# Optimization experiments

Measured on AMD Instinct MI355X. Metric: run time of the kernel, lower is better.

Reference implementation:

```python
import jax, jax.numpy as jnp
import numpy as np

STATE_MASS = 4.0
EPS = 1e-5
LOW_RANK_SCALE = 0.1  # _LOW_RANK_SCALE_INIT


def _ln(x, g, b):
    mu = jnp.mean(x, axis=-1, keepdims=True)
    var = jnp.var(x, axis=-1, keepdims=True)
    return (x - mu) * jax.lax.rsqrt(var + EPS) * g + b


def _signed_abs_softmax(s, axis=-1):
    s = jnp.nan_to_num(s)
    return jnp.sign(s) * jax.nn.softmax(jnp.abs(s), axis=axis)


def _signed_softmax_state(st):
    st = jnp.nan_to_num(st)
    return jnp.sign(st) * jax.nn.softmax(jnp.abs(st), axis=-1) * STATE_MASS


def _low_rank_scores(dst, src, Ut_w, Ut_b, Us_w, Us_b, w):
    # bilinear low-rank pairwise: score[b,i,j] = sum_r (dst_i Ut)_r * w_r * (src_j Us)_r
    pt = dst @ Ut_w + Ut_b                      # [B,Nd,R]
    ps = src @ Us_w + Us_b                      # [B,Ns,R]
    return jnp.einsum('bir,r,bjr->bij', pt, w * LOW_RANK_SCALE, ps)


def _gather_rows(x, idx):
    # x: [B,N,...], idx: [B,M,K] -> [B,M,K,...] (per-batch gather, no NxM broadcast)
    return jax.vmap(lambda xi, ii: xi[ii])(x, idx)


def setup_inputs() -> dict:
    key = jax.random.key(0)
    ks = jax.random.split(key, 8)
    B, S, D, M, R = 16, 2048, 512, 256, 64
    std = 0.02
    return {
        'token_val': jax.random.normal(ks[0], (B, S, D), jnp.float32),
        'token_state': jax.random.normal(ks[1], (B, S), jnp.float32),
        'init_state': jax.random.normal(ks[2], (M,), jnp.float32) * std,
        'init_val': jax.random.normal(ks[3], (M, D), jnp.float32) * std,
        'rUs_w': jax.random.normal(ks[4], (D, R), jnp.float32) * std,
        'rUs_b': jnp.zeros((R,), jnp.float32),
        'rUt_w': jax.random.normal(ks[5], (D, R), jnp.float32) * std,
        'rUt_b': jnp.zeros((R,), jnp.float32),
        'r_w': jnp.ones((R,), jnp.float32),
        'pUs_w': jax.random.normal(ks[6], (D, R), jnp.float32) * std,
        'pUs_b': jnp.zeros((R,), jnp.float32),
        'pUt_w': jax.random.normal(ks[7], (D, R), jnp.float32) * std,
        'pUt_b': jnp.zeros((R,), jnp.float32),
        'p_w': jnp.ones((R,), jnp.float32),
        'ln_g': jnp.ones((D,), jnp.float32),
        'ln_b': jnp.zeros((D,), jnp.float32),
        'topk': 16,
    }


def reference(token_val, token_state, init_state, init_val,
              rUs_w, rUs_b, rUt_w, rUt_b, r_w,
              pUs_w, pUs_b, pUt_w, pUt_b, p_w,
              ln_g, ln_b, topk):
    B = token_val.shape[0]
    M, D = init_val.shape

    # _MemoryLevel.initialize
    mem_state = _signed_softmax_state(jnp.broadcast_to(init_state, (B, M)))
    mem_val = _ln(jnp.broadcast_to(init_val, (B, M, D)), ln_g, ln_b)

    # ---- SparseTransition (write): route tokens -> slots, top-k sources/slot ----
    scores = _low_rank_scores(mem_val, token_val, rUt_w, rUt_b, rUs_w, rUs_b, r_w)  # [B,M,S]
    _, idx = jax.lax.top_k(jnp.abs(scores), topk)              # [B,M,K]
    sel = jnp.take_along_axis(scores, idx, axis=-1)            # [B,M,K]
    edges = _signed_abs_softmax(sel, axis=-1)                  # signed-abs-softmax over edges
    v_sel = _gather_rows(token_val, idx)                       # [B,M,K,D]
    s_sel = _gather_rows(token_state, idx)                     # [B,M,K]
    mem_val = mem_val + jnp.einsum('bmk,bmkd->bmd', edges, v_sel)   # merge_mode='add'
    mem_state = mem_state + jnp.einsum('bmk,bmk->bm', edges, s_sel)
    mem_state = _signed_softmax_state(mem_state)
    mem_val = _ln(mem_val, ln_g, ln_b)

    # ---- SparsePropagation within slots: state-weighted top-k edges, residual ----
    pscores = _low_rank_scores(mem_val, mem_val, pUt_w, pUt_b, pUs_w, pUs_b, p_w)   # [B,M,M]
    pscores = pscores * mem_state[:, None, :]                  # state_weight_edges
    _, pidx = jax.lax.top_k(jnp.abs(pscores), topk)            # [B,M,K]
    psel = jnp.take_along_axis(pscores, pidx, axis=-1)
    pe = _signed_abs_softmax(psel, axis=-1)
    pv = _gather_rows(mem_val, pidx)                           # [B,M,K,D]
    pst = _gather_rows(mem_state, pidx)                        # [B,M,K]
    mem_val = mem_val + jnp.einsum('bmk,bmkd->bmd', pe, pv)    # residual=True
    mem_state = mem_state + jnp.einsum('bmk,bmk->bm', pe, pst)
    mem_state = _signed_softmax_state(mem_state)
    mem_val = _ln(mem_val, ln_g, ln_b)
    return mem_val
```

## Files before the change

kernel.cpp:

```cpp
#include <hip/hip_runtime.h>
#include <hip/hip_bf16.h>
#include <math.h>

#define BB 16
#define SS 2048
#define DD 512
#define MM 256
#define RR 64
#define KK 16
#define GPAD 68

__device__ __forceinline__ float wave_sum(float v) {
#pragma unroll
  for (int off = 32; off > 0; off >>= 1) v += __shfl_xor(v, off);
  return v;
}

__device__ __forceinline__ float sgnf(float v) {
  return (v > 0.f) ? 1.f : ((v < 0.f) ? -1.f : 0.f);
}

__global__ __launch_bounds__(256) void k_init(
    const float* __restrict__ init_val, const float* __restrict__ ln_g,
    const float* __restrict__ ln_b, const float* __restrict__ rUt_w,
    const float* __restrict__ rUt_b, const float* __restrict__ r_w,
    float* __restrict__ mv0, float* __restrict__ pt0) {
  int m = blockIdx.x, t = threadIdx.x;
  __shared__ float row[DD];
  __shared__ float red[8];
  float x0 = init_val[m * DD + t];
  float x1 = init_val[m * DD + t + 256];
  float s = wave_sum(x0 + x1);
  float sq = wave_sum(x0 * x0 + x1 * x1);
  if ((t & 63) == 0) { red[t >> 6] = s; red[4 + (t >> 6)] = sq; }
  __syncthreads();
  float mean = (red[0] + red[1] + red[2] + red[3]) * (1.0f / DD);
  float var = (red[4] + red[5] + red[6] + red[7]) * (1.0f / DD) - mean * mean;
  float rs = rsqrtf(var + 1e-5f);
  float n0 = (x0 - mean) * rs * ln_g[t] + ln_b[t];
  float n1 = (x1 - mean) * rs * ln_g[t + 256] + ln_b[t + 256];
  mv0[m * DD + t] = n0;
  mv0[m * DD + t + 256] = n1;
  row[t] = n0;
  row[t + 256] = n1;
  __syncthreads();
  if (t < RR) {
    float acc = rUt_b[t];
    for (int d = 0; d < DD; ++d) acc += row[d] * rUt_w[d * RR + t];
    pt0[m * RR + t] = acc * r_w[t] * 0.1f;
  }
}

__global__ __launch_bounds__(256) void k_state_softmax(
    const float* __restrict__ in, float* __restrict__ out) {
  int b = blockIdx.x, t = threadIdx.x;
  __shared__ float red[4];
  float v = in[b * MM + t];
  float a = fabsf(v);
  float mx = a;
#pragma unroll
  for (int off = 32; off > 0; off >>= 1) mx = fmaxf(mx, __shfl_xor(mx, off));
  if ((t & 63) == 0) red[t >> 6] = mx;
  __syncthreads();
  mx = fmaxf(fmaxf(red[0], red[1]), fmaxf(red[2], red[3]));
  __syncthreads();
  float e = expf(a - mx);
  float ssum = wave_sum(e);
  if ((t & 63) == 0) red[t >> 6] = ssum;
  __syncthreads();
  ssum = red[0] + red[1] + red[2] + red[3];
  out[b * MM + t] = sgnf(v) * e / ssum * 4.0f;
}

__global__ __launch_bounds__(256) void k_ps(
    const float* __restrict__ A, const float* __restrict__ W,
    const float* __restrict__ bias, float* __restrict__ C) {
  __shared__ float Ast[32][128];
  __shared__ float Ws[32][RR];
  int t = threadIdx.x;
  int tx = t & 15;
  int ty = t >> 4;
  int row0 = blockIdx.x * 128;
  float4 ra[4];
  float4 rw[2];
#pragma unroll
  for (int i = 0; i < 4; ++i) {
    int slot = i * 256 + t;
    int r = slot >> 3, k4 = slot & 7;
    ra[i] = *reinterpret_cast<const float4*>(&A[(size_t)(row0 + r) * DD + k4 * 4]);
  }
#pragma unroll
  for (int i = 0; i < 2; ++i) {
    int slot = i * 256 + t;
    int k = slot >> 4, c4 = slot & 15;
    rw[i] = *reinterpret_cast<const float4*>(&W[(size_t)k * RR + c4 * 4]);
  }
  float acc[8][4] = {};
  for (int c = 0; c < 16; ++c) {
    __syncthreads();
#pragma unroll
    for (int i = 0; i < 4; ++i) {
      int slot = i * 256 + t;
      int r = slot >> 3, k4 = slot & 7;
      Ast[k4 * 4 + 0][r] = ra[i].x;
      Ast[k4 * 4 + 1][r] = ra[i].y;
      Ast[k4 * 4 + 2][r] = ra[i].z;
      Ast[k4 * 4 + 3][r] = ra[i].w;
    }
#pragma unroll
    for (int i = 0; i < 2; ++i) {
      int slot = i * 256 + t;
      int k = slot >> 4, c4 = slot & 15;
      *reinterpret_cast<float4*>(&Ws[k][c4 * 4]) = rw[i];
    }
    __syncthreads();
    if (c < 15) {
      int kc = (c + 1) * 32;
#pragma unroll
      for (int i = 0; i < 4; ++i) {
        int slot = i * 256 + t;
        int r = slot >> 3, k4 = slot & 7;
        ra[i] = *reinterpret_cast<const float4*>(
            &A[(size_t)(row0 + r) * DD + kc + k4 * 4]);
      }
#pragma unroll
      for (int i = 0; i < 2; ++i) {
        int slot = i * 256 + t;
        int k = slot >> 4, c4 = slot & 15;
        rw[i] = *reinterpret_cast<const float4*>(
            &W[(size_t)(kc + k) * RR + c4 * 4]);
      }
    }
#pragma unroll
    for (int k = 0; k < 32; ++k) {
      float4 alo = *reinterpret_cast<const float4*>(&Ast[k][ty * 8]);
      float4 ahi = *reinterpret_cast<const float4*>(&Ast[k][ty * 8 + 4]);
      float4 w4 = *reinterpret_cast<const float4*>(&Ws[k][tx * 4]);
      acc[0][0] += alo.x * w4.x; acc[0][1] += alo.x * w4.y; acc[0][2] += alo.x * w4.z; acc[0][3] += alo.x * w4.w;
      acc[1][0] += alo.y * w4.x; acc[1][1] += alo.y * w4.y; acc[1][2] += alo.y * w4.z; acc[1][3] += alo.y * w4.w;
      acc[2][0] += alo.z * w4.x; acc[2][1] += alo.z * w4.y; acc[2][2] += alo.z * w4.z; acc[2][3] += alo.z * w4.w;
      acc[3][0] += alo.w * w4.x; acc[3][1] += alo.w * w4.y; acc[3][2] += alo.w * w4.z; acc[3][3] += alo.w * w4.w;
      acc[4][0] += ahi.x * w4.x; acc[4][1] += ahi.x * w4.y; acc[4][2] += ahi.x * w4.z; acc[4][3] += ahi.x * w4.w;
      acc[5][0] += ahi.y * w4.x; acc[5][1] += ahi.y * w4.y; acc[5][2] += ahi.y * w4.z; acc[5][3] += ahi.y * w4.w;
      acc[6][0] += ahi.z * w4.x; acc[6][1] += ahi.z * w4.y; acc[6][2] += ahi.z * w4.z; acc[6][3] += ahi.z * w4.w;
      acc[7][0] += ahi.w * w4.x; acc[7][1] += ahi.w * w4.y; acc[7][2] += ahi.w * w4.z; acc[7][3] += ahi.w * w4.w;
    }
  }
  float4 bv = *reinterpret_cast<const float4*>(&bias[tx * 4]);
#pragma unroll
  for (int r = 0; r < 8; ++r) {
    int rr = row0 + ty * 8 + r;
    float4 o;
    o.x = acc[r][0] + bv.x; o.y = acc[r][1] + bv.y;
    o.z = acc[r][2] + bv.z; o.w = acc[r][3] + bv.w;
    *reinterpret_cast<float4*>(&C[(size_t)rr * RR + tx * 4]) = o;
  }
}

template <bool TRANS_OUT>
__device__ __forceinline__ void gemm_body(
    const float* __restrict__ A, const float* __restrict__ W,
    const float* __restrict__ bias, const float* __restrict__ colscale,
    float csmul, const float* __restrict__ rowscale, float* __restrict__ C,
    int row0, float (*Ast)[GPAD], float (*Ws)[GPAD]) {
  int tid = threadIdx.x;
  int ty = tid >> 4, tx = tid & 15;
  float acc[4][4] = {};
  for (int kc = 0; kc < DD; kc += 32) {
#pragma unroll
    for (int i = 0; i < 2; ++i) {
      int s4 = i * 256 + tid;
      int r = s4 >> 3;
      int k4 = s4 & 7;
      float4 v = *reinterpret_cast<const float4*>(
          &A[(size_t)(row0 + r) * DD + kc + k4 * 4]);
      Ast[k4 * 4 + 0][r] = v.x;
      Ast[k4 * 4 + 1][r] = v.y;
      Ast[k4 * 4 + 2][r] = v.z;
      Ast[k4 * 4 + 3][r] = v.w;
    }
#pragma unroll
    for (int i = 0; i < 2; ++i) {
      int s4 = i * 256 + tid;
      int r = s4 >> 4;
      int c4 = s4 & 15;
      float4 v = *reinterpret_cast<const float4*>(
          &W[(size_t)(kc + r) * RR + c4 * 4]);
      *reinterpret_cast<float4*>(&Ws[r][c4 * 4]) = v;
    }
    __syncthreads();
#pragma unroll
    for (int k = 0; k < 32; ++k) {
      float4 a4 = *reinterpret_cast<const float4*>(&Ast[k][ty * 4]);
      float4 w4 = *reinterpret_cast<const float4*>(&Ws[k][tx * 4]);
      acc[0][0] += a4.x * w4.x; acc[0][1] += a4.x * w4.y;
      acc[0][2] += a4.x * w4.z; acc[0][3] += a4.x * w4.w;
      acc[1][0] += a4.y * w4.x; acc[1][1] += a4.y * w4.y;
      acc[1][2] += a4.y * w4.z; acc[1][3] += a4.y * w4.w;
      acc[2][0] += a4.z * w4.x; acc[2][1] += a4.z * w4.y;
      acc[2][2] += a4.z * w4.z; acc[2][3] += a4.z * w4.w;
      acc[3][0] += a4.w * w4.x; acc[3][1] += a4.w * w4.y;
      acc[3][2] += a4.w * w4.z; acc[3][3] += a4.w * w4.w;
    }
    __syncthreads();
  }
#pragma unroll
  for (int i = 0; i < 4; ++i) {
    int rr = row0 + ty * 4 + i;
    float rsc = rowscale ? rowscale[rr] : 1.f;
#pragma unroll
    for (int j = 0; j < 4; ++j) {
      int cc = tx * 4 + j;
      float v = acc[i][j] + bias[cc];
      if (colscale) v *= colscale[cc] * csmul;
      v *= rsc;
      if (TRANS_OUT) {
        C[((size_t)(rr >> 8) * RR + cc) * MM + (rr & 255)] = v;
      } else {
        C[(size_t)rr * RR + cc] = v;
      }
    }
  }
}

__global__ __launch_bounds__(256) void k_gemm_pair(
    const float* __restrict__ mv1, const float* __restrict__ pUt_w,
    const float* __restrict__ pUt_b, const float* __restrict__ p_w,
    const float* __restrict__ pUs_w, const float* __restrict__ pUs_b,
    const float* __restrict__ ms1, float* __restrict__ pt1,
    float* __restrict__ ps1T) {
  __shared__ float Ast[32][GPAD];
  __shared__ float Ws[32][GPAD];
  if (blockIdx.x < 64) {
    gemm_body<false>(mv1, pUt_w, pUt_b, p_w, 0.1f, nullptr, pt1,
                     blockIdx.x * 64, Ast, Ws);
  } else {
    gemm_body<true>(mv1, pUs_w, pUs_b, nullptr, 1.f, ms1, ps1T,
                    (blockIdx.x - 64) * 64, Ast, Ws);
  }
}

#define PSW 144
__device__ __forceinline__ int psw(int j) { return j + ((j >> 5) << 2); }

__global__ __launch_bounds__(256) void k_scores(
    const float* __restrict__ pt0, const float* __restrict__ ps,
    float* __restrict__ scores) {
  __shared__ float PtT[RR][64];
  __shared__ float PsT[RR][PSW];
  int t = threadIdx.x;
  int b = blockIdx.z;
  int m0 = blockIdx.y * 64;
  int j0 = blockIdx.x * 128;
  {
    int tm4 = t >> 4, tk4 = t & 15;
    const float* base = pt0 + (size_t)(m0 + tm4 * 4) * RR + tk4 * 4;
    float4 v0 = *reinterpret_cast<const float4*>(base);
    float4 v1 = *reinterpret_cast<const float4*>(base + RR);
    float4 v2 = *reinterpret_cast<const float4*>(base + 2 * RR);
    float4 v3 = *reinterpret_cast<const float4*>(base + 3 * RR);
    float4 w;
    w.x = v0.x; w.y = v1.x; w.z = v2.x; w.w = v3.x;
    *reinterpret_cast<float4*>(&PtT[tk4 * 4 + 0][tm4 * 4]) = w;
    w.x = v0.y; w.y = v1.y; w.z = v2.y; w.w = v3.y;
    *reinterpret_cast<float4*>(&PtT[tk4 * 4 + 1][tm4 * 4]) = w;
    w.x = v0.z; w.y = v1.z; w.z = v2.z; w.w = v3.z;
    *reinterpret_cast<float4*>(&PtT[tk4 * 4 + 2][tm4 * 4]) = w;
    w.x = v0.w; w.y = v1.w; w.z = v2.w; w.w = v3.w;
    *reinterpret_cast<float4*>(&PtT[tk4 * 4 + 3][tm4 * 4]) = w;
  }
#pragma unroll
  for (int ii = 0; ii < 2; ++ii) {
    int slot = ii * 256 + t;
    int jt = slot >> 4, kt = slot & 15;
    const float* base = ps + ((size_t)b * SS + j0 + jt * 4) * RR + kt * 4;
    float4 v0 = *reinterpret_cast<const float4*>(base);
    float4 v1 = *reinterpret_cast<const float4*>(base + RR);
    float4 v2 = *reinterpret_cast<const float4*>(base + 2 * RR);
    float4 v3 = *reinterpret_cast<const float4*>(base + 3 * RR);
    int jc = psw(jt * 4);
    float4 w;
    w.x = v0.x; w.y = v1.x; w.z = v2.x; w.w = v3.x;
    *reinterpret_cast<float4*>(&PsT[kt * 4 + 0][jc]) = w;
    w.x = v0.y; w.y = v1.y; w.z = v2.y; w.w = v3.y;
    *reinterpret_cast<float4*>(&PsT[kt * 4 + 1][jc]) = w;
    w.x = v0.z; w.y = v1.z; w.z = v2.z; w.w = v3.z;
    *reinterpret_cast<float4*>(&PsT[kt * 4 + 2][jc]) = w;
    w.x = v0.w; w.y = v1.w; w.z = v2.w; w.w = v3.w;
    *reinterpret_cast<float4*>(&PsT[kt * 4 + 3][jc]) = w;
  }
  __syncthreads();
  int tj = t & 15;
  int tm = t >> 4;
  int jlo = psw(tj * 8);
  int jhi = psw(tj * 8 + 4);
  float acc[4][8] = {};
#pragma unroll
  for (int k = 0; k < RR; ++k) {
    float4 a4 = *reinterpret_cast<const float4*>(&PtT[k][tm * 4]);
    float4 w0 = *reinterpret_cast<const float4*>(&PsT[k][jlo]);
    float4 w1 = *reinterpret_cast<const float4*>(&PsT[k][jhi]);
    acc[0][0] += a4.x * w0.x; acc[0][1] += a4.x * w0.y; acc[0][2] += a4.x * w0.z; acc[0][3] += a4.x * w0.w;
    acc[0][4] += a4.x * w1.x; acc[0][5] += a4.x * w1.y; acc[0][6] += a4.x * w1.z; acc[0][7] += a4.x * w1.w;
    acc[1][0] += a4.y * w0.x; acc[1][1] += a4.y * w0.y; acc[1][2] += a4.y * w0.z; acc[1][3] += a4.y * w0.w;
    acc[1][4] += a4.y * w1.x; acc[1][5] += a4.y * w1.y; acc[1][6] += a4.y * w1.z; acc[1][7] += a4.y * w1.w;
    acc[2][0] += a4.z * w0.x; acc[2][1] += a4.z * w0.y; acc[2][2] += a4.z * w0.z; acc[2][3] += a4.z * w0.w;
    acc[2][4] += a4.z * w1.x; acc[2][5] += a4.z * w1.y; acc[2][6] += a4.z * w1.z; acc[2][7] += a4.z * w1.w;
    acc[3][0] += a4.w * w0.x; acc[3][1] += a4.w * w0.y; acc[3][2] += a4.w * w0.z; acc[3][3] += a4.w * w0.w;
    acc[3][4] += a4.w * w1.x; acc[3][5] += a4.w * w1.y; acc[3][6] += a4.w * w1.z; acc[3][7] += a4.w * w1.w;
  }
  float* obase = scores + (size_t)b * MM * SS + (size_t)(m0 + tm * 4) * SS + j0 + tj * 8;
#pragma unroll
  for (int i = 0; i < 4; ++i) {
    float4 o0, o1;
    o0.x = acc[i][0]; o0.y = acc[i][1]; o0.z = acc[i][2]; o0.w = acc[i][3];
    o1.x = acc[i][4]; o1.y = acc[i][5]; o1.z = acc[i][6]; o1.w = acc[i][7];
    *reinterpret_cast<float4*>(obase + (size_t)i * SS) = o0;
    *reinterpret_cast<float4*>(obase + (size_t)i * SS + 4) = o1;
  }
}

__global__ __launch_bounds__(256) void k_write(
    const float* __restrict__ scores, const float* __restrict__ token_val,
    const float* __restrict__ token_state, const float* __restrict__ mv0,
    const float* __restrict__ ms0, const float* __restrict__ ln_g,
    const float* __restrict__ ln_b, float* __restrict__ mv1,
    float* __restrict__ ms_w) {
  int t = threadIdx.x;
  int wave = t >> 6, lane = t & 63;
  int i = blockIdx.x;
  int slot = i >> 3;
  int b = 2 * (i & 7) + (slot >> 6);
  int m = (slot & 63) * 4 + wave;
  int row = b * MM + m;
  __shared__ float srl[4][SS];
  __shared__ int selj_sh[4][KK];
  float4* srl4 = reinterpret_cast<float4*>(&srl[wave][0]);
  const float* srow = scores + (size_t)row * SS;
  unsigned maxa = 0u;
#pragma unroll
  for (int ch = 0; ch < 8; ++ch) {
    float4 q = *reinterpret_cast<const float4*>(srow + (ch * 64 + lane) * 4);
    srl4[ch * 64 + lane] = q;
    maxa = max(maxa, __float_as_uint(q.x) & 0x7fffffffu);
    maxa = max(maxa, __float_as_uint(q.y) & 0x7fffffffu);
    maxa = max(maxa, __float_as_uint(q.z) & 0x7fffffffu);
    maxa = max(maxa, __float_as_uint(q.w) & 0x7fffffffu);
  }
#pragma unroll
  for (int off = 32; off > 0; off >>= 1)
    maxa = max(maxa, (unsigned)__shfl_xor((int)maxa, off));
  unsigned lo = 0u, hi = maxa, thr = 0u;
  bool early = false;
  while (lo < hi) {
    unsigned mid = lo + ((hi - lo + 1u) >> 1);
    int cnt = 0;
#pragma unroll
    for (int ch = 0; ch < 8; ++ch) {
      float4 q = srl4[ch * 64 + lane];
      cnt += __popcll(__ballot((__float_as_uint(q.x) & 0x7fffffffu) >= mid));
      cnt += __popcll(__ballot((__float_as_uint(q.y) & 0x7fffffffu) >= mid));
      cnt += __popcll(__ballot((__float_as_uint(q.z) & 0x7fffffffu) >= mid));
      cnt += __popcll(__ballot((__float_as_uint(q.w) & 0x7fffffffu) >= mid));
    }
    if (cnt == KK) { thr = mid; early = true; break; }
    if (cnt > KK) lo = mid; else hi = mid - 1u;
  }
  if (!early) thr = lo;
  unsigned long long ltmask = (1ull << lane) - 1ull;
  int s = 0;
  unsigned tiemask = 0u;
#pragma unroll
  for (int ch = 0; ch < 8; ++ch) {
    float4 q = srl4[ch * 64 + lane];
    unsigned a4[4] = {__float_as_uint(q.x) & 0x7fffffffu,
                      __float_as_uint(q.y) & 0x7fffffffu,
                      __float_as_uint(q.z) & 0x7fffffffu,
                      __float_as_uint(q.w) & 0x7fffffffu};
#pragma unroll
    for (int cc = 0; cc < 4; ++cc) {
      bool sg = early ? (a4[cc] >= thr) : (a4[cc] > thr);
      unsigned long long mk = __ballot(sg);
      if (sg) selj_sh[wave][s + __popcll(mk & ltmask)] = ch * 256 + lane * 4 + cc;
      s += __popcll(mk);
      if (!early && a4[cc] == thr) tiemask |= 1u << (ch * 4 + cc);
    }
  }
  int taken = s;
  while (taken < KK) {
    int myj = 0x7fffffff;
#pragma unroll
    for (int c = 0; c < 32; ++c)
      if ((tiemask >> c) & 1u) {
        int j = (c >> 2) * 256 + lane * 4 + (c & 3);
        myj = min(myj, j);
      }
    int wj = myj;
#pragma unroll
    for (int off = 32; off > 0; off >>= 1) wj = min(wj, __shfl_xor(wj, off));
    if (wj == 0x7fffffff) break;
    if (((wj >> 2) & 63) == lane) tiemask &= ~(1u << (((wj >> 8) << 2) | (wj & 3)));
    if (lane == 0) selj_sh[wave][taken] = wj;
    ++taken;
  }
  int js[KK];
  float es[KK];
#pragma unroll
  for (int k = 0; k < KK; ++k) {
    js[k] = selj_sh[wave][k];
    es[k] = srl[wave][js[k]];
  }
  float mx = 0.f;
#pragma unroll
  for (int k = 0; k < KK; ++k) mx = fmaxf(mx, fabsf(es[k]));
  float ssum = 0.f;
#pragma unroll
  for (int k = 0; k < KK; ++k) {
    float ex = expf(fabsf(es[k]) - mx);
    ssum += ex;
    es[k] = sgnf(es[k]) * ex;
  }
  float inv = 1.f / ssum;
  int dbase = lane * 8;
  const float* m0row = mv0 + m * DD + dbase;
  float4 a0 = *reinterpret_cast<const float4*>(m0row);
  float4 a1 = *reinterpret_cast<const float4*>(m0row + 4);
  float acc[8] = {a0.x, a0.y, a0.z, a0.w, a1.x, a1.y, a1.z, a1.w};
  float stacc = 0.f;
#pragma unroll
  for (int k = 0; k < KK; ++k) {
    float e = es[k] * inv;
    const float* tv = token_val + ((size_t)b * SS + js[k]) * DD + dbase;
    float4 u0 = *reinterpret_cast<const float4*>(tv);
    float4 u1 = *reinterpret_cast<const float4*>(tv + 4);
    acc[0] += e * u0.x; acc[1] += e * u0.y; acc[2] += e * u0.z; acc[3] += e * u0.w;
    acc[4] += e * u1.x; acc[5] += e * u1.y; acc[6] += e * u1.z; acc[7] += e * u1.w;
    stacc += e * token_state[(size_t)b * SS + js[k]];
  }
  if (lane == 0) ms_w[row] = ms0[m] + stacc;
  float s1 = 0.f, s2 = 0.f;
#pragma unroll
  for (int c = 0; c < 8; ++c) { s1 += acc[c]; s2 += acc[c] * acc[c]; }
  s1 = wave_sum(s1);
  s2 = wave_sum(s2);
  float mean = s1 * (1.0f / DD);
  float var = s2 * (1.0f / DD) - mean * mean;
  float rs = rsqrtf(var + 1e-5f);
  float4 g0 = *reinterpret_cast<const float4*>(ln_g + dbase);
  float4 g1 = *reinterpret_cast<const float4*>(ln_g + dbase + 4);
  float4 b0v = *reinterpret_cast<const float4*>(ln_b + dbase);
  float4 b1v = *reinterpret_cast<const float4*>(ln_b + dbase + 4);
  float4 o0, o1;
  o0.x = (acc[0] - mean) * rs * g0.x + b0v.x;
  o0.y = (acc[1] - mean) * rs * g0.y + b0v.y;
  o0.z = (acc[2] - mean) * rs * g0.z + b0v.z;
  o0.w = (acc[3] - mean) * rs * g0.w + b0v.w;
  o1.x = (acc[4] - mean) * rs * g1.x + b1v.x;
  o1.y = (acc[5] - mean) * rs * g1.y + b1v.y;
  o1.z = (acc[6] - mean) * rs * g1.z + b1v.z;
  o1.w = (acc[7] - mean) * rs * g1.w + b1v.w;
  float* orow = mv1 + (size_t)row * DD + dbase;
  *reinterpret_cast<float4*>(orow) = o0;
  *reinterpret_cast<float4*>(orow + 4) = o1;
}

__global__ __launch_bounds__(256, 4) void k_prop(
    const float* __restrict__ pt1, const float* __restrict__ ps1T,
    const float* __restrict__ mv1, const float* __restrict__ ln_g,
    const float* __restrict__ ln_b, float* __restrict__ out) {
  int t = threadIdx.x;
  int wave = t >> 6, lane = t & 63;
  int row = blockIdx.x * 4 + wave;
  int b = row >> 8, m = row & 255;
  __shared__ int selj_sh[4][KK];
  __shared__ float selv_sh[4][KK];
  float ptval = pt1[(size_t)row * RR + lane];
  const float* pB = ps1T + (size_t)b * RR * MM + lane * 4;
  float sc[4] = {0.f, 0.f, 0.f, 0.f};
#pragma unroll 8
  for (int r = 0; r < RR; ++r) {
    float w = __shfl(ptval, r);
    float4 pv = *reinterpret_cast<const float4*>(pB + r * MM);
    sc[0] += w * pv.x; sc[1] += w * pv.y; sc[2] += w * pv.z; sc[3] += w * pv.w;
  }
  int jbase = lane * 4;
  unsigned au[4];
#pragma unroll
  for (int c = 0; c < 4; ++c) au[c] = __float_as_uint(sc[c]) & 0x7fffffffu;
  unsigned lo = 0u, hi = 0x7f800000u, thr = 0u;
  bool early = false;
  while (lo < hi) {
    unsigned mid = lo + ((hi - lo + 1u) >> 1);
    int cnt = 0;
#pragma unroll
    for (int c = 0; c < 4; ++c) cnt += __popcll(__ballot(au[c] >= mid));
    if (cnt == KK) { thr = mid; early = true; break; }
    if (cnt > KK) lo = mid; else hi = mid - 1u;
  }
  if (!early) thr = lo;
  unsigned long long ltmask = (1ull << lane) - 1ull;
  int s = 0;
  unsigned tiemask = 0u;
#pragma unroll
  for (int c = 0; c < 4; ++c) {
    bool sg = early ? (au[c] >= thr) : (au[c] > thr);
    unsigned long long mk = __ballot(sg);
    if (sg) {
      int slot = s + __popcll(mk & ltmask);
      selj_sh[wave][slot] = jbase + c;
      selv_sh[wave][slot] = sc[c];
    }
    s += __popcll(mk);
    if (!early && au[c] == thr) tiemask |= 1u << c;
  }
  int taken = s;
  while (taken < KK) {
    int myj = 0x7fffffff;
#pragma unroll
    for (int c = 0; c < 4; ++c)
      if ((tiemask >> c) & 1u) myj = min(myj, jbase + c);
    int wj = myj;
#pragma unroll
    for (int off = 32; off > 0; off >>= 1) wj = min(wj, __shfl_xor(wj, off));
    if (wj == 0x7fffffff) break;
    if (wj >= jbase && wj < jbase + 4) {
      tiemask &= ~(1u << (wj - jbase));
      selv_sh[wave][taken] = sc[wj - jbase];
      if (lane == (wj >> 2)) selj_sh[wave][taken] = wj;
    }
    ++taken;
  }
  int js[KK];
  float es[KK];
#pragma unroll
  for (int k = 0; k < KK; ++k) { js[k] = selj_sh[wave][k]; es[k] = selv_sh[wave][k]; }
  float mx = 0.f;
#pragma unroll
  for (int k = 0; k < KK; ++k) mx = fmaxf(mx, fabsf(es[k]));
  float ssum = 0.f;
#pragma unroll
  for (int k = 0; k < KK; ++k) {
    float ex = expf(fabsf(es[k]) - mx);
    ssum += ex;
    es[k] = sgnf(es[k]) * ex;
  }
  float inv = 1.f / ssum;
  int dbase = lane * 8;
  const float* mrow = mv1 + (size_t)row * DD + dbase;
  float4 a0 = *reinterpret_cast<const float4*>(mrow);
  float4 a1 = *reinterpret_cast<const float4*>(mrow + 4);
  float acc[8] = {a0.x, a0.y, a0.z, a0.w, a1.x, a1.y, a1.z, a1.w};
#pragma unroll
  for (int k = 0; k < KK; ++k) {
    float e = es[k] * inv;
    const float* pv = mv1 + ((size_t)b * MM + js[k]) * DD + dbase;
    float4 u0 = *reinterpret_cast<const float4*>(pv);
    float4 u1 = *reinterpret_cast<const float4*>(pv + 4);
    acc[0] += e * u0.x; acc[1] += e * u0.y; acc[2] += e * u0.z; acc[3] += e * u0.w;
    acc[4] += e * u1.x; acc[5] += e * u1.y; acc[6] += e * u1.z; acc[7] += e * u1.w;
  }
  float s1 = 0.f, s2 = 0.f;
#pragma unroll
  for (int c = 0; c < 8; ++c) { s1 += acc[c]; s2 += acc[c] * acc[c]; }
  s1 = wave_sum(s1);
  s2 = wave_sum(s2);
  float mean = s1 * (1.0f / DD);
  float var = s2 * (1.0f / DD) - mean * mean;
  float rs = rsqrtf(var + 1e-5f);
  float4 g0 = *reinterpret_cast<const float4*>(ln_g + dbase);
  float4 g1 = *reinterpret_cast<const float4*>(ln_g + dbase + 4);
  float4 b0v = *reinterpret_cast<const float4*>(ln_b + dbase);
  float4 b1v = *reinterpret_cast<const float4*>(ln_b + dbase + 4);
  float4 o0, o1;
  o0.x = (acc[0] - mean) * rs * g0.x + b0v.x;
  o0.y = (acc[1] - mean) * rs * g0.y + b0v.y;
  o0.z = (acc[2] - mean) * rs * g0.z + b0v.z;
  o0.w = (acc[3] - mean) * rs * g0.w + b0v.w;
  o1.x = (acc[4] - mean) * rs * g1.x + b1v.x;
  o1.y = (acc[5] - mean) * rs * g1.y + b1v.y;
  o1.z = (acc[6] - mean) * rs * g1.z + b1v.z;
  o1.w = (acc[7] - mean) * rs * g1.w + b1v.w;
  float* orow = out + (size_t)row * DD + dbase;
  *reinterpret_cast<float4*>(orow) = o0;
  *reinterpret_cast<float4*>(orow + 4) = o1;
}

extern "C" void kernel_launch(void* const* d_in, const int* in_sizes, int n_in,
                              void* d_out, int out_size, void* d_ws,
                              size_t ws_size, hipStream_t stream) {
  const float* token_val = (const float*)d_in[0];
  const float* token_state = (const float*)d_in[1];
  const float* init_state = (const float*)d_in[2];
  const float* init_val = (const float*)d_in[3];
  const float* rUs_w = (const float*)d_in[4];
  const float* rUs_b = (const float*)d_in[5];
  const float* rUt_w = (const float*)d_in[6];
  const float* rUt_b = (const float*)d_in[7];
  const float* r_w = (const float*)d_in[8];
  const float* pUs_w = (const float*)d_in[9];
  const float* pUs_b = (const float*)d_in[10];
  const float* pUt_w = (const float*)d_in[11];
  const float* pUt_b = (const float*)d_in[12];
  const float* p_w = (const float*)d_in[13];
  const float* ln_g = (const float*)d_in[14];
  const float* ln_b = (const float*)d_in[15];
  float* out = (float*)d_out;

  float* ws = (float*)d_ws;
  float* mv0 = ws;    ws += MM * DD;
  float* pt0 = ws;    ws += MM * RR;
  float* ms0 = ws;    ws += MM;
  float* ps = ws;     ws += (size_t)BB * SS * RR;
  float* scores = ws; ws += (size_t)BB * MM * SS;
  float* mv1 = ws;    ws += (size_t)BB * MM * DD;
  float* ms_w = ws;   ws += BB * MM;
  float* ms1 = ws;    ws += BB * MM;
  float* pt1 = ws;    ws += (size_t)BB * MM * RR;
  float* ps1T = ws;   ws += (size_t)BB * RR * MM;

  k_init<<<MM, 256, 0, stream>>>(init_val, ln_g, ln_b, rUt_w, rUt_b, r_w, mv0, pt0);
  k_state_softmax<<<1, 256, 0, stream>>>(init_state, ms0);
  k_ps<<<(BB * SS) / 128, 256, 0, stream>>>(token_val, rUs_w, rUs_b, ps);
  dim3 gs(SS / 128, MM / 64, BB);
  k_scores<<<gs, 256, 0, stream>>>(pt0, ps, scores);
  k_write<<<(BB * MM) / 4, 256, 0, stream>>>(scores, token_val, token_state,
                                             mv0, ms0, ln_g, ln_b, mv1, ms_w);
  k_state_softmax<<<BB, 256, 0, stream>>>(ms_w, ms1);
  k_gemm_pair<<<128, 256, 0, stream>>>(mv1, pUt_w, pUt_b, p_w, pUs_w, pUs_b,
                                       ms1, pt1, ps1T);
  k_prop<<<(BB * MM) / 4, 256, 0, stream>>>(pt1, ps1T, mv1, ln_g, ln_b, out);
}
```

Measured before the change: 173.8 us.

## Split k_ps reduction over two K halves and sum partials in k_scores

The token projection GEMM is split along the D dimension into two halves, doubling the grid from 256 to 512 blocks so more CUs are busy. The two partial results are written to separate buffers (the second reusing mv1 workspace) and summed when k_scores loads them. The A-tile load mapping is also changed so a wave reads consecutive rows instead of consecutive columns. The cost is an extra 8 MB partial buffer written and read, plus doubled loads in k_scores.

```diff
diff --git a/kernel.cpp b/kernel.cpp
--- a/kernel.cpp
+++ b/kernel.cpp
@@ -74,34 +74,41 @@
 
 __global__ __launch_bounds__(256) void k_ps(
     const float* __restrict__ A, const float* __restrict__ W,
-    const float* __restrict__ bias, float* __restrict__ C) {
+    const float* __restrict__ bias, float* __restrict__ C0,
+    float* __restrict__ C1) {
   __shared__ float Ast[32][128];
   __shared__ float Ws[32][RR];
   int t = threadIdx.x;
+  int lane = t & 63;
+  int wv = t >> 6;
   int tx = t & 15;
   int ty = t >> 4;
-  int row0 = blockIdx.x * 128;
+  int half = blockIdx.x >> 8;
+  int row0 = (blockIdx.x & 255) * 128;
+  int k0 = half * 256;
+  float* C = half ? C1 : C0;
   float4 ra[4];
   float4 rw[2];
 #pragma unroll
   for (int i = 0; i < 4; ++i) {
-    int slot = i * 256 + t;
-    int r = slot >> 3, k4 = slot & 7;
-    ra[i] = *reinterpret_cast<const float4*>(&A[(size_t)(row0 + r) * DD + k4 * 4]);
+    int r = (i & 1) * 64 + lane;
+    int k4 = (i >> 1) * 4 + wv;
+    ra[i] = *reinterpret_cast<const float4*>(
+        &A[(size_t)(row0 + r) * DD + k0 + k4 * 4]);
   }
 #pragma unroll
   for (int i = 0; i < 2; ++i) {
     int slot = i * 256 + t;
     int k = slot >> 4, c4 = slot & 15;
-    rw[i] = *reinterpret_cast<const float4*>(&W[(size_t)k * RR + c4 * 4]);
+    rw[i] = *reinterpret_cast<const float4*>(&W[(size_t)(k0 + k) * RR + c4 * 4]);
   }
   float acc[8][4] = {};
-  for (int c = 0; c < 16; ++c) {
+  for (int c = 0; c < 8; ++c) {
     __syncthreads();
 #pragma unroll
     for (int i = 0; i < 4; ++i) {
-      int slot = i * 256 + t;
-      int r = slot >> 3, k4 = slot & 7;
+      int r = (i & 1) * 64 + lane;
+      int k4 = (i >> 1) * 4 + wv;
       Ast[k4 * 4 + 0][r] = ra[i].x;
       Ast[k4 * 4 + 1][r] = ra[i].y;
       Ast[k4 * 4 + 2][r] = ra[i].z;
@@ -114,12 +121,12 @@
       *reinterpret_cast<float4*>(&Ws[k][c4 * 4]) = rw[i];
     }
     __syncthreads();
-    if (c < 15) {
-      int kc = (c + 1) * 32;
+    if (c < 7) {
+      int kc = k0 + (c + 1) * 32;
 #pragma unroll
       for (int i = 0; i < 4; ++i) {
-        int slot = i * 256 + t;
-        int r = slot >> 3, k4 = slot & 7;
+        int r = (i & 1) * 64 + lane;
+        int k4 = (i >> 1) * 4 + wv;
         ra[i] = *reinterpret_cast<const float4*>(
             &A[(size_t)(row0 + r) * DD + kc + k4 * 4]);
       }
@@ -146,7 +153,12 @@
       acc[7][0] += ahi.w * w4.x; acc[7][1] += ahi.w * w4.y; acc[7][2] += ahi.w * w4.z; acc[7][3] += ahi.w * w4.w;
     }
   }
-  float4 bv = *reinterpret_cast<const float4*>(&bias[tx * 4]);
+  float4 bv;
+  if (half == 0) {
+    bv = *reinterpret_cast<const float4*>(&bias[tx * 4]);
+  } else {
+    bv.x = bv.y = bv.z = bv.w = 0.f;
+  }
 #pragma unroll
   for (int r = 0; r < 8; ++r) {
     int rr = row0 + ty * 8 + r;
@@ -244,8 +256,8 @@
 __device__ __forceinline__ int psw(int j) { return j + ((j >> 5) << 2); }
 
 __global__ __launch_bounds__(256) void k_scores(
-    const float* __restrict__ pt0, const float* __restrict__ ps,
-    float* __restrict__ scores) {
+    const float* __restrict__ pt0, const float* __restrict__ ps0,
+    const float* __restrict__ ps1, float* __restrict__ scores) {
   __shared__ float PtT[RR][64];
   __shared__ float PsT[RR][PSW];
   int t = threadIdx.x;
@@ -273,11 +285,21 @@
   for (int ii = 0; ii < 2; ++ii) {
     int slot = ii * 256 + t;
     int jt = slot >> 4, kt = slot & 15;
-    const float* base = ps + ((size_t)b * SS + j0 + jt * 4) * RR + kt * 4;
-    float4 v0 = *reinterpret_cast<const float4*>(base);
-    float4 v1 = *reinterpret_cast<const float4*>(base + RR);
-    float4 v2 = *reinterpret_cast<const float4*>(base + 2 * RR);
-    float4 v3 = *reinterpret_cast<const float4*>(base + 3 * RR);
+    size_t off = ((size_t)b * SS + j0 + jt * 4) * RR + kt * 4;
+    const float* base0 = ps0 + off;
+    const float* base1 = ps1 + off;
+    float4 v0 = *reinterpret_cast<const float4*>(base0);
+    float4 v1 = *reinterpret_cast<const float4*>(base0 + RR);
+    float4 v2 = *reinterpret_cast<const float4*>(base0 + 2 * RR);
+    float4 v3 = *reinterpret_cast<const float4*>(base0 + 3 * RR);
+    float4 u0 = *reinterpret_cast<const float4*>(base1);
+    float4 u1 = *reinterpret_cast<const float4*>(base1 + RR);
+    float4 u2 = *reinterpret_cast<const float4*>(base1 + 2 * RR);
+    float4 u3 = *reinterpret_cast<const float4*>(base1 + 3 * RR);
+    v0.x += u0.x; v0.y += u0.y; v0.z += u0.z; v0.w += u0.w;
+    v1.x += u1.x; v1.y += u1.y; v1.z += u1.z; v1.w += u1.w;
+    v2.x += u2.x; v2.y += u2.y; v2.z += u2.z; v2.w += u2.w;
+    v3.x += u3.x; v3.y += u3.y; v3.z += u3.z; v3.w += u3.w;
     int jc = psw(jt * 4);
     float4 w;
     w.x = v0.x; w.y = v1.x; w.z = v2.x; w.w = v3.x;
@@ -617,12 +639,13 @@
   float* ms1 = ws;    ws += BB * MM;
   float* pt1 = ws;    ws += (size_t)BB * MM * RR;
   float* ps1T = ws;   ws += (size_t)BB * RR * MM;
+  float* psB = mv1;
 
   k_init<<<MM, 256, 0, stream>>>(init_val, ln_g, ln_b, rUt_w, rUt_b, r_w, mv0, pt0);
   k_state_softmax<<<1, 256, 0, stream>>>(init_state, ms0);
-  k_ps<<<(BB * SS) / 128, 256, 0, stream>>>(token_val, rUs_w, rUs_b, ps);
+  k_ps<<<512, 256, 0, stream>>>(token_val, rUs_w, rUs_b, ps, psB);
   dim3 gs(SS / 128, MM / 64, BB);
-  k_scores<<<gs, 256, 0, stream>>>(pt0, ps, scores);
+  k_scores<<<gs, 256, 0, stream>>>(pt0, ps, psB, scores);
   k_write<<<(BB * MM) / 4, 256, 0, stream>>>(scores, token_val, token_state,
                                              mv0, ms0, ln_g, ln_b, mv1, ms_w);
   k_state_softmax<<<BB, 256, 0, stream>>>(ms_w, ms1);
```

After: 164.2 us. -5.5%, faster.
